# Performance work log

Measured on AMD Instinct MI355X. Metric: run time of the kernel, lower is better.

Reference implementation:

```python
import jax, jax.numpy as jnp
import numpy as np

C_IN = 64
C_QK = C_IN // 8  # 8


def setup_inputs() -> dict:
    key = jax.random.key(0)
    ks = jax.random.split(key, 8)
    B, C, D, H, W = 2, C_IN, 8, 32, 32
    x = jax.random.normal(ks[0], (B, C, D, H, W), dtype=jnp.float32)
    s = 1.0 / np.sqrt(C)
    Wq = jax.random.normal(ks[1], (C_QK, C), dtype=jnp.float32) * s
    bq = jax.random.normal(ks[2], (C_QK,), dtype=jnp.float32) * 0.01
    Wk = jax.random.normal(ks[3], (C_QK, C), dtype=jnp.float32) * s
    bk = jax.random.normal(ks[4], (C_QK,), dtype=jnp.float32) * 0.01
    Wv = jax.random.normal(ks[5], (C, C), dtype=jnp.float32) * s
    bv = jax.random.normal(ks[6], (C,), dtype=jnp.float32) * 0.01
    gamma = jax.random.normal(ks[7], (1,), dtype=jnp.float32) * 0.1
    return {"x": x, "Wq": Wq, "bq": bq, "Wk": Wk, "bk": bk,
            "Wv": Wv, "bv": bv, "gamma": gamma}


def reference(x, Wq, bq, Wk, bk, Wv, bv, gamma):
    B, C, D, H, W = x.shape
    N = D * H * W
    xf = x.reshape(B, C, N)  # flatten spatial dims (D,H,W order)
    # 1x1x1 conv3d == per-position channel matmul
    q = jnp.einsum('oc,bcn->bno', Wq, xf) + bq            # [B, N, Cqk]
    k = jnp.einsum('oc,bcn->bon', Wk, xf) + bk[:, None]   # [B, Cqk, N]
    v = jnp.einsum('oc,bcn->bon', Wv, xf) + bv[:, None]   # [B, C, N]
    energy = jnp.einsum('bnc,bcm->bnm', q, k)             # [B, N, N] (unscaled)
    attn = jax.nn.softmax(energy, axis=-1)
    # out[b,c,m] = sum_n v[b,c,n] * attn[b,m,n]  (bmm with attention^T)
    out = jnp.einsum('bcn,bmn->bcm', v, attn)
    out = out.reshape(B, C, D, H, W)
    return gamma[0] * out + x
```

## Files before the change

kernel.cpp:

```cpp
#include <hip/hip_runtime.h>
#include <hip/hip_bf16.h>
#include <math.h>

#define NPOS 8192
#define CIN 64
#define CQK 8
#define NB 2
#define LOG2E 1.4426950408889634f
#define SOFF 16.0f

typedef __attribute__((ext_vector_type(8))) short bf16x8;
typedef __attribute__((ext_vector_type(16))) float f32x16;

__device__ __forceinline__ unsigned short f2bf(float f) {
  union { float f; unsigned int u; } a; a.f = f;
  unsigned int r = a.u + 0x7FFFu + ((a.u >> 16) & 1u);
  return (unsigned short)(r >> 16);
}

__global__ __launch_bounds__(256, 2) void qkv_proj(
    const float* __restrict__ x,
    const float* __restrict__ Wq, const float* __restrict__ bq,
    const float* __restrict__ Wk, const float* __restrict__ bk,
    const float* __restrict__ Wv, const float* __restrict__ bv,
    unsigned short* __restrict__ Qb, unsigned short* __restrict__ Kb,
    unsigned short* __restrict__ VB) {
  __shared__ float sWq[CQK * CIN], sWk[CQK * CIN], sWv[CIN * CIN], sb[2 * CQK + CIN];
  __shared__ unsigned short sV[32][66];
  int t = threadIdx.x;
  for (int i = t; i < CQK * CIN; i += 256) { sWq[i] = Wq[i] * LOG2E; sWk[i] = Wk[i]; }
  for (int i = t; i < CIN * CIN; i += 256) sWv[i] = Wv[i];
  if (t < CQK) sb[t] = bq[t] * LOG2E;
  if (t >= CQK && t < 2 * CQK) sb[t] = bk[t - CQK];
  if (t >= 2 * CQK && t < 2 * CQK + CIN) sb[t] = bv[t - 2 * CQK];
  __syncthreads();

  int p_loc = t & 31, grp = t >> 5;
  int gid = blockIdx.x * 32 + p_loc;
  int b = gid >> 13;
  int n = gid & (NPOS - 1);
  const float* xp = x + (size_t)b * CIN * NPOS + n;
  float xv[CIN];
#pragma unroll
  for (int c = 0; c < CIN; ++c) xv[c] = xp[(size_t)c * NPOS];

  {
    int o = grp;
    float aq = sb[o], ak = sb[CQK + o];
    const float4* wq4 = (const float4*)&sWq[o * CIN];
    const float4* wk4 = (const float4*)&sWk[o * CIN];
#pragma unroll
    for (int c4 = 0; c4 < 16; ++c4) {
      float4 wq = wq4[c4], wk = wk4[c4];
      float x0 = xv[4 * c4], x1 = xv[4 * c4 + 1], x2 = xv[4 * c4 + 2], x3 = xv[4 * c4 + 3];
      aq += wq.x * x0 + wq.y * x1 + wq.z * x2 + wq.w * x3;
      ak += wk.x * x0 + wk.y * x1 + wk.z * x2 + wk.w * x3;
    }
    Qb[(size_t)gid * CQK + o] = f2bf(aq);
    Kb[(size_t)gid * CQK + o] = f2bf(ak);
  }
#pragma unroll
  for (int oo = 0; oo < 8; ++oo) {
    int o = grp * 8 + oo;
    float av = sb[2 * CQK + o];
    const float4* wv4 = (const float4*)&sWv[o * CIN];
#pragma unroll
    for (int c4 = 0; c4 < 16; ++c4) {
      float4 w = wv4[c4];
      av += w.x * xv[4 * c4] + w.y * xv[4 * c4 + 1] + w.z * xv[4 * c4 + 2] + w.w * xv[4 * c4 + 3];
    }
    sV[p_loc][o] = f2bf(av);
  }
  __syncthreads();

  {
    int gid0 = blockIdx.x * 32;
    int bb = gid0 >> 13;
    int jb = (gid0 & (NPOS - 1)) >> 5;
    int f = t >> 6;
    int ln = t & 63;
    int ch = ((f >> 1) << 5) + (ln & 31);
    int w0 = ((f & 1) << 4) + (((ln >> 5) & 1) << 2);
    union { unsigned short s[8]; bf16x8 v; } ou;
#pragma unroll
    for (int i = 0; i < 8; ++i) {
      int p = w0 + (i & 3) + (((i >> 2) & 1) << 3);
      ou.s[i] = sV[p][ch];
    }
    *reinterpret_cast<bf16x8*>(
        VB + (((size_t)bb * 256 + jb) * 2048 + (size_t)f * 512 + ln * 8)) = ou.v;
  }
}

__global__ __launch_bounds__(512, 2) void flash_attn(
    const unsigned short* __restrict__ Qb, const unsigned short* __restrict__ Kb,
    const unsigned short* __restrict__ VB, const float* __restrict__ x,
    const float* __restrict__ gamma, float* __restrict__ out) {
  int tid = threadIdx.x;
  int wave = tid >> 6, lane = tid & 63;
  int qcol = lane & 31, hi = lane >> 5;
  int blk = blockIdx.x;
  int b = blk >> 7, qt = blk & 127;
  int qbase = qt * 64;

  bf16x8 qfrag0, qfrag1;
#pragma unroll
  for (int i = 0; i < 8; ++i) { qfrag0[i] = 0; qfrag1[i] = 0; }
  if (!hi) {
    qfrag0 = *reinterpret_cast<const bf16x8*>(Qb + ((size_t)b * NPOS + qbase + qcol) * CQK);
    qfrag1 = *reinterpret_cast<const bf16x8*>(Qb + ((size_t)b * NPOS + qbase + 32 + qcol) * CQK);
  }

  f32x16 z;
#pragma unroll
  for (int i = 0; i < 16; ++i) z[i] = -SOFF;
  f32x16 accA0, accB0, accA1, accB1;
#pragma unroll
  for (int i = 0; i < 16; ++i) { accA0[i] = 0.f; accB0[i] = 0.f; accA1[i] = 0.f; accB1[i] = 0.f; }
  float l0 = 0.f, l1 = 0.f;

  const unsigned short* Kp = Kb + (size_t)b * NPOS * CQK;
  const bf16x8* Vt = reinterpret_cast<const bf16x8*>(VB + (size_t)b * 256 * 2048);

  int jb0 = wave << 5;
  bf16x8 kcur = *reinterpret_cast<const bf16x8*>(Kp + ((size_t)(jb0 << 5) + qcol) * CQK);

  for (int tt = 0; tt < 32; ++tt) {
    const bf16x8* tile = Vt + (size_t)(jb0 + tt) * 256;
    bf16x8 va0 = tile[lane];
    bf16x8 va1 = tile[64 + lane];
    bf16x8 vb0 = tile[128 + lane];
    bf16x8 vb1 = tile[192 + lane];

    f32x16 S0 = __builtin_amdgcn_mfma_f32_32x32x16_bf16(kcur, qfrag0, z, 0, 0, 0);
    f32x16 S1 = __builtin_amdgcn_mfma_f32_32x32x16_bf16(kcur, qfrag1, z, 0, 0, 0);

    int jn = jb0 + ((tt + 1) & 31);
    bf16x8 knx = *reinterpret_cast<const bf16x8*>(Kp + ((size_t)(jn << 5) + qcol) * CQK);

    unsigned int pk0[8], pk1[8];
    float lsa = 0.f, lsb = 0.f, lsc = 0.f, lsd = 0.f;
#pragma unroll
    for (int jj = 0; jj < 8; ++jj) {
      float pa = __builtin_amdgcn_exp2f(S0[2 * jj]);
      float pb = __builtin_amdgcn_exp2f(S0[2 * jj + 1]);
      float pc = __builtin_amdgcn_exp2f(S1[2 * jj]);
      float pd = __builtin_amdgcn_exp2f(S1[2 * jj + 1]);
      lsa += pa; lsb += pb; lsc += pc; lsd += pd;
      pk0[jj] = __builtin_amdgcn_perm(__float_as_uint(pb), __float_as_uint(pa), 0x07060302u);
      pk1[jj] = __builtin_amdgcn_perm(__float_as_uint(pd), __float_as_uint(pc), 0x07060302u);
    }
    l0 += lsa + lsb;
    l1 += lsc + lsd;

    union { unsigned int ui[4]; bf16x8 v; } PA00, PA10, PA01, PA11;
    PA00.ui[0] = pk0[0]; PA00.ui[1] = pk0[1]; PA00.ui[2] = pk0[2]; PA00.ui[3] = pk0[3];
    PA10.ui[0] = pk0[4]; PA10.ui[1] = pk0[5]; PA10.ui[2] = pk0[6]; PA10.ui[3] = pk0[7];
    PA01.ui[0] = pk1[0]; PA01.ui[1] = pk1[1]; PA01.ui[2] = pk1[2]; PA01.ui[3] = pk1[3];
    PA11.ui[0] = pk1[4]; PA11.ui[1] = pk1[5]; PA11.ui[2] = pk1[6]; PA11.ui[3] = pk1[7];

    accA0 = __builtin_amdgcn_mfma_f32_32x32x16_bf16(va0, PA00.v, accA0, 0, 0, 0);
    accA0 = __builtin_amdgcn_mfma_f32_32x32x16_bf16(va1, PA10.v, accA0, 0, 0, 0);
    accB0 = __builtin_amdgcn_mfma_f32_32x32x16_bf16(vb0, PA00.v, accB0, 0, 0, 0);
    accB0 = __builtin_amdgcn_mfma_f32_32x32x16_bf16(vb1, PA10.v, accB0, 0, 0, 0);
    accA1 = __builtin_amdgcn_mfma_f32_32x32x16_bf16(va0, PA01.v, accA1, 0, 0, 0);
    accA1 = __builtin_amdgcn_mfma_f32_32x32x16_bf16(va1, PA11.v, accA1, 0, 0, 0);
    accB1 = __builtin_amdgcn_mfma_f32_32x32x16_bf16(vb0, PA01.v, accB1, 0, 0, 0);
    accB1 = __builtin_amdgcn_mfma_f32_32x32x16_bf16(vb1, PA11.v, accB1, 0, 0, 0);

    kcur = knx;
  }

  __shared__ float sL[8][64];
  __shared__ float sLinv[64];
  __shared__ float sacc[64][68];
  float lp0 = l0 + __shfl_xor(l0, 32);
  float lp1 = l1 + __shfl_xor(l1, 32);
  if (!hi) { sL[wave][qcol] = lp0; sL[wave][32 + qcol] = lp1; }
  __syncthreads();
  if (tid < 64) {
    float L = 0.f;
#pragma unroll
    for (int w2 = 0; w2 < 8; ++w2) L += sL[w2][tid];
    sLinv[tid] = 1.0f / L;
  }

  for (int w2 = 0; w2 < 8; ++w2) {
    __syncthreads();
    if (wave == w2) {
#pragma unroll
      for (int k = 0; k < 4; ++k) {
        int c0 = (k << 3) + (hi << 2);
        float4 cA0 = make_float4(accA0[4 * k], accA0[4 * k + 1], accA0[4 * k + 2], accA0[4 * k + 3]);
        float4 cB0 = make_float4(accB0[4 * k], accB0[4 * k + 1], accB0[4 * k + 2], accB0[4 * k + 3]);
        float4 cA1 = make_float4(accA1[4 * k], accA1[4 * k + 1], accA1[4 * k + 2], accA1[4 * k + 3]);
        float4 cB1 = make_float4(accB1[4 * k], accB1[4 * k + 1], accB1[4 * k + 2], accB1[4 * k + 3]);
        float4* pA0 = (float4*)&sacc[qcol][c0];
        float4* pB0 = (float4*)&sacc[qcol][c0 + 32];
        float4* pA1 = (float4*)&sacc[32 + qcol][c0];
        float4* pB1 = (float4*)&sacc[32 + qcol][c0 + 32];
        if (w2 == 0) { *pA0 = cA0; *pB0 = cB0; *pA1 = cA1; *pB1 = cB1; }
        else {
          float4 a = *pA0, bb = *pB0, c = *pA1, d = *pB1;
          a.x += cA0.x; a.y += cA0.y; a.z += cA0.z; a.w += cA0.w;
          bb.x += cB0.x; bb.y += cB0.y; bb.z += cB0.z; bb.w += cB0.w;
          c.x += cA1.x; c.y += cA1.y; c.z += cA1.z; c.w += cA1.w;
          d.x += cB1.x; d.y += cB1.y; d.z += cB1.z; d.w += cB1.w;
          *pA0 = a; *pB0 = bb; *pA1 = c; *pB1 = d;
        }
      }
    }
  }
  __syncthreads();

  float g = gamma[0];
  for (int i = tid; i < CIN * 64; i += 512) {
    int c = i >> 6, q = i & 63;
    size_t idx = ((size_t)b * CIN + c) * NPOS + qbase + q;
    out[idx] = g * sacc[q][c] * sLinv[q] + x[idx];
  }
}

extern "C" void kernel_launch(void* const* d_in, const int* in_sizes, int n_in,
                              void* d_out, int out_size, void* d_ws, size_t ws_size,
                              hipStream_t stream) {
  const float* x     = (const float*)d_in[0];
  const float* Wq    = (const float*)d_in[1];
  const float* bq    = (const float*)d_in[2];
  const float* Wk    = (const float*)d_in[3];
  const float* bk    = (const float*)d_in[4];
  const float* Wv    = (const float*)d_in[5];
  const float* bv    = (const float*)d_in[6];
  const float* gamma = (const float*)d_in[7];
  float* out = (float*)d_out;

  unsigned short* Qb = (unsigned short*)d_ws;
  unsigned short* Kb = Qb + (size_t)NB * NPOS * CQK;
  unsigned short* VB = Kb + (size_t)NB * NPOS * CQK;

  qkv_proj<<<dim3(NB * NPOS / 32), dim3(256), 0, stream>>>(
      x, Wq, bq, Wk, bk, Wv, bv, Qb, Kb, VB);
  flash_attn<<<dim3(NB * NPOS / 64), dim3(512), 0, stream>>>(
      Qb, Kb, VB, x, gamma, out);
}
```

Baseline: 45.26 us.

## Fuse QKV projection and flash attention into one cooperative kernel with grid sync

Merges the projection kernel and the attention kernel into a single cooperative launch. Each 512-thread block projects 64 positions into Q/K/V workspace, then a grid-wide barrier separates the projection from the attention phase. This removes one kernel launch and the gap between kernels. In exchange it adds a grid-sync cost, requires all 256 blocks to be co-resident, and raises shared memory use per block.

```diff
diff --git a/kernel.cpp b/kernel.cpp
--- a/kernel.cpp
+++ b/kernel.cpp
@@ -1,6 +1,9 @@
 #include <hip/hip_runtime.h>
 #include <hip/hip_bf16.h>
+#include <hip/hip_cooperative_groups.h>
 #include <math.h>
+
+namespace cg = cooperative_groups;
 
 #define NPOS 8192
 #define CIN 64
@@ -18,84 +21,87 @@
   return (unsigned short)(r >> 16);
 }
 
-__global__ __launch_bounds__(256, 2) void qkv_proj(
+__global__ __launch_bounds__(512, 2) void pam_fused(
     const float* __restrict__ x,
     const float* __restrict__ Wq, const float* __restrict__ bq,
     const float* __restrict__ Wk, const float* __restrict__ bk,
     const float* __restrict__ Wv, const float* __restrict__ bv,
+    const float* __restrict__ gamma, float* __restrict__ out,
     unsigned short* __restrict__ Qb, unsigned short* __restrict__ Kb,
     unsigned short* __restrict__ VB) {
   __shared__ float sWq[CQK * CIN], sWk[CQK * CIN], sWv[CIN * CIN], sb[2 * CQK + CIN];
-  __shared__ unsigned short sV[32][66];
-  int t = threadIdx.x;
-  for (int i = t; i < CQK * CIN; i += 256) { sWq[i] = Wq[i] * LOG2E; sWk[i] = Wk[i]; }
-  for (int i = t; i < CIN * CIN; i += 256) sWv[i] = Wv[i];
-  if (t < CQK) sb[t] = bq[t] * LOG2E;
-  if (t >= CQK && t < 2 * CQK) sb[t] = bk[t - CQK];
-  if (t >= 2 * CQK && t < 2 * CQK + CIN) sb[t] = bv[t - 2 * CQK];
-  __syncthreads();
-
-  int p_loc = t & 31, grp = t >> 5;
-  int gid = blockIdx.x * 32 + p_loc;
-  int b = gid >> 13;
-  int n = gid & (NPOS - 1);
-  const float* xp = x + (size_t)b * CIN * NPOS + n;
-  float xv[CIN];
-#pragma unroll
-  for (int c = 0; c < CIN; ++c) xv[c] = xp[(size_t)c * NPOS];
-
+  __shared__ unsigned short sV[64][66];
   {
-    int o = grp;
-    float aq = sb[o], ak = sb[CQK + o];
-    const float4* wq4 = (const float4*)&sWq[o * CIN];
-    const float4* wk4 = (const float4*)&sWk[o * CIN];
-#pragma unroll
-    for (int c4 = 0; c4 < 16; ++c4) {
-      float4 wq = wq4[c4], wk = wk4[c4];
-      float x0 = xv[4 * c4], x1 = xv[4 * c4 + 1], x2 = xv[4 * c4 + 2], x3 = xv[4 * c4 + 3];
-      aq += wq.x * x0 + wq.y * x1 + wq.z * x2 + wq.w * x3;
-      ak += wk.x * x0 + wk.y * x1 + wk.z * x2 + wk.w * x3;
-    }
-    Qb[(size_t)gid * CQK + o] = f2bf(aq);
-    Kb[(size_t)gid * CQK + o] = f2bf(ak);
-  }
-#pragma unroll
-  for (int oo = 0; oo < 8; ++oo) {
-    int o = grp * 8 + oo;
-    float av = sb[2 * CQK + o];
-    const float4* wv4 = (const float4*)&sWv[o * CIN];
-#pragma unroll
-    for (int c4 = 0; c4 < 16; ++c4) {
-      float4 w = wv4[c4];
-      av += w.x * xv[4 * c4] + w.y * xv[4 * c4 + 1] + w.z * xv[4 * c4 + 2] + w.w * xv[4 * c4 + 3];
-    }
-    sV[p_loc][o] = f2bf(av);
-  }
-  __syncthreads();
-
-  {
-    int gid0 = blockIdx.x * 32;
-    int bb = gid0 >> 13;
-    int jb = (gid0 & (NPOS - 1)) >> 5;
-    int f = t >> 6;
-    int ln = t & 63;
-    int ch = ((f >> 1) << 5) + (ln & 31);
-    int w0 = ((f & 1) << 4) + (((ln >> 5) & 1) << 2);
-    union { unsigned short s[8]; bf16x8 v; } ou;
-#pragma unroll
-    for (int i = 0; i < 8; ++i) {
-      int p = w0 + (i & 3) + (((i >> 2) & 1) << 3);
-      ou.s[i] = sV[p][ch];
-    }
-    *reinterpret_cast<bf16x8*>(
-        VB + (((size_t)bb * 256 + jb) * 2048 + (size_t)f * 512 + ln * 8)) = ou.v;
-  }
-}
-
-__global__ __launch_bounds__(512, 2) void flash_attn(
-    const unsigned short* __restrict__ Qb, const unsigned short* __restrict__ Kb,
-    const unsigned short* __restrict__ VB, const float* __restrict__ x,
-    const float* __restrict__ gamma, float* __restrict__ out) {
+    int t = threadIdx.x;
+    for (int i = t; i < CQK * CIN; i += 512) { sWq[i] = Wq[i] * LOG2E; sWk[i] = Wk[i]; }
+    for (int i = t; i < CIN * CIN; i += 512) sWv[i] = Wv[i];
+    if (t < CQK) sb[t] = bq[t] * LOG2E;
+    if (t >= CQK && t < 2 * CQK) sb[t] = bk[t - CQK];
+    if (t >= 2 * CQK && t < 2 * CQK + CIN) sb[t] = bv[t - 2 * CQK];
+    __syncthreads();
+
+    int p_loc = t & 63, grp = t >> 6;
+    int gid = blockIdx.x * 64 + p_loc;
+    int b = gid >> 13;
+    int n = gid & (NPOS - 1);
+    const float* xp = x + (size_t)b * CIN * NPOS + n;
+    float xv[CIN];
+#pragma unroll
+    for (int c = 0; c < CIN; ++c) xv[c] = xp[(size_t)c * NPOS];
+
+    {
+      int o = grp;
+      float aq = sb[o], ak = sb[CQK + o];
+      const float4* wq4 = (const float4*)&sWq[o * CIN];
+      const float4* wk4 = (const float4*)&sWk[o * CIN];
+#pragma unroll
+      for (int c4 = 0; c4 < 16; ++c4) {
+        float4 wq = wq4[c4], wk = wk4[c4];
+        float x0 = xv[4 * c4], x1 = xv[4 * c4 + 1], x2 = xv[4 * c4 + 2], x3 = xv[4 * c4 + 3];
+        aq += wq.x * x0 + wq.y * x1 + wq.z * x2 + wq.w * x3;
+        ak += wk.x * x0 + wk.y * x1 + wk.z * x2 + wk.w * x3;
+      }
+      Qb[(size_t)gid * CQK + o] = f2bf(aq);
+      Kb[(size_t)gid * CQK + o] = f2bf(ak);
+    }
+#pragma unroll
+    for (int oo = 0; oo < 8; ++oo) {
+      int o = grp * 8 + oo;
+      float av = sb[2 * CQK + o];
+      const float4* wv4 = (const float4*)&sWv[o * CIN];
+#pragma unroll
+      for (int c4 = 0; c4 < 16; ++c4) {
+        float4 w = wv4[c4];
+        av += w.x * xv[4 * c4] + w.y * xv[4 * c4 + 1] + w.z * xv[4 * c4 + 2] + w.w * xv[4 * c4 + 3];
+      }
+      sV[p_loc][o] = f2bf(av);
+    }
+    __syncthreads();
+
+    {
+      int gid0 = blockIdx.x * 64;
+      int bb = gid0 >> 13;
+      int jb0 = (gid0 & (NPOS - 1)) >> 5;
+      int cc = t;
+      int jbl = cc >> 8;
+      int rem = cc & 255;
+      int f = rem >> 6;
+      int ln = rem & 63;
+      int ch = ((f >> 1) << 5) + (ln & 31);
+      int w0 = ((f & 1) << 4) + (((ln >> 5) & 1) << 2);
+      union { unsigned short s[8]; bf16x8 v; } ou;
+#pragma unroll
+      for (int i = 0; i < 8; ++i) {
+        int p = (jbl << 5) + w0 + (i & 3) + (((i >> 2) & 1) << 3);
+        ou.s[i] = sV[p][ch];
+      }
+      *reinterpret_cast<bf16x8*>(
+          VB + (((size_t)bb * 256 + jb0 + jbl) * 2048 + (size_t)f * 512 + ln * 8)) = ou.v;
+    }
+  }
+
+  cg::this_grid().sync();
+
   int tid = threadIdx.x;
   int wave = tid >> 6, lane = tid & 63;
   int qcol = lane & 31, hi = lane >> 5;
@@ -238,8 +244,9 @@
   unsigned short* Kb = Qb + (size_t)NB * NPOS * CQK;
   unsigned short* VB = Kb + (size_t)NB * NPOS * CQK;
 
-  qkv_proj<<<dim3(NB * NPOS / 32), dim3(256), 0, stream>>>(
-      x, Wq, bq, Wk, bk, Wv, bv, Qb, Kb, VB);
-  flash_attn<<<dim3(NB * NPOS / 64), dim3(512), 0, stream>>>(
-      Qb, Kb, VB, x, gamma, out);
+  void* args[] = {(void*)&x, (void*)&Wq, (void*)&bq, (void*)&Wk, (void*)&bk,
+                  (void*)&Wv, (void*)&bv, (void*)&gamma, (void*)&out,
+                  (void*)&Qb, (void*)&Kb, (void*)&VB};
+  hipLaunchCooperativeKernel((void*)pam_fused, dim3(NB * NPOS / 64), dim3(512),
+                             args, 0, stream);
 }
```

Measured after the change: 81.26 us. 79.5% more time.

## Replace exp2 with bit-trick approximation and compute row sums via MFMA

Applied to the files above, without the earlier changes.

Replaces the hardware exp2 in the softmax loop with a Schraudolph-style approximation: an FMA scales and biases the score, and the float-to-uint conversion yields the IEEE bit pattern, whose top 16 bits are packed straight into bf16. It also drops the per-lane scalar accumulation of softmax denominators and instead computes row sums with extra MFMAs against a vector of bf16 ones. This cuts transcendental and VALU work per tile but adds four MFMAs per iteration, and the exp approximation is far less accurate (piecewise-linear mantissa), which could hurt numerical correctness.

```diff
diff --git a/kernel.cpp b/kernel.cpp
--- a/kernel.cpp
+++ b/kernel.cpp
@@ -8,6 +8,8 @@
 #define NB 2
 #define LOG2E 1.4426950408889634f
 #define SOFF 16.0f
+#define EXP2_SCALE 8388608.0f
+#define EXP2_BIAS  1065173216.0f
 
 typedef __attribute__((ext_vector_type(8))) short bf16x8;
 typedef __attribute__((ext_vector_type(16))) float f32x16;
@@ -111,13 +113,20 @@
     qfrag1 = *reinterpret_cast<const bf16x8*>(Qb + ((size_t)b * NPOS + qbase + 32 + qcol) * CQK);
   }
 
+  bf16x8 ones;
+#pragma unroll
+  for (int i = 0; i < 8; ++i) ones[i] = (short)0x3F80;
+
   f32x16 z;
 #pragma unroll
   for (int i = 0; i < 16; ++i) z[i] = -SOFF;
   f32x16 accA0, accB0, accA1, accB1;
-#pragma unroll
-  for (int i = 0; i < 16; ++i) { accA0[i] = 0.f; accB0[i] = 0.f; accA1[i] = 0.f; accB1[i] = 0.f; }
-  float l0 = 0.f, l1 = 0.f;
+  f32x16 accL0, accL1;
+#pragma unroll
+  for (int i = 0; i < 16; ++i) {
+    accA0[i] = 0.f; accB0[i] = 0.f; accA1[i] = 0.f; accB1[i] = 0.f;
+    accL0[i] = 0.f; accL1[i] = 0.f;
+  }
 
   const unsigned short* Kp = Kb + (size_t)b * NPOS * CQK;
   const bf16x8* Vt = reinterpret_cast<const bf16x8*>(VB + (size_t)b * 256 * 2048);
@@ -139,19 +148,15 @@
     bf16x8 knx = *reinterpret_cast<const bf16x8*>(Kp + ((size_t)(jn << 5) + qcol) * CQK);
 
     unsigned int pk0[8], pk1[8];
-    float lsa = 0.f, lsb = 0.f, lsc = 0.f, lsd = 0.f;
 #pragma unroll
     for (int jj = 0; jj < 8; ++jj) {
-      float pa = __builtin_amdgcn_exp2f(S0[2 * jj]);
-      float pb = __builtin_amdgcn_exp2f(S0[2 * jj + 1]);
-      float pc = __builtin_amdgcn_exp2f(S1[2 * jj]);
-      float pd = __builtin_amdgcn_exp2f(S1[2 * jj + 1]);
-      lsa += pa; lsb += pb; lsc += pc; lsd += pd;
-      pk0[jj] = __builtin_amdgcn_perm(__float_as_uint(pb), __float_as_uint(pa), 0x07060302u);
-      pk1[jj] = __builtin_amdgcn_perm(__float_as_uint(pd), __float_as_uint(pc), 0x07060302u);
-    }
-    l0 += lsa + lsb;
-    l1 += lsc + lsd;
+      unsigned int ua = (unsigned int)fmaf(S0[2 * jj],     EXP2_SCALE, EXP2_BIAS);
+      unsigned int ub = (unsigned int)fmaf(S0[2 * jj + 1], EXP2_SCALE, EXP2_BIAS);
+      unsigned int uc = (unsigned int)fmaf(S1[2 * jj],     EXP2_SCALE, EXP2_BIAS);
+      unsigned int ud = (unsigned int)fmaf(S1[2 * jj + 1], EXP2_SCALE, EXP2_BIAS);
+      pk0[jj] = __builtin_amdgcn_perm(ub, ua, 0x07060302u);
+      pk1[jj] = __builtin_amdgcn_perm(ud, uc, 0x07060302u);
+    }
 
     union { unsigned int ui[4]; bf16x8 v; } PA00, PA10, PA01, PA11;
     PA00.ui[0] = pk0[0]; PA00.ui[1] = pk0[1]; PA00.ui[2] = pk0[2]; PA00.ui[3] = pk0[3];
@@ -167,6 +172,10 @@
     accA1 = __builtin_amdgcn_mfma_f32_32x32x16_bf16(va1, PA11.v, accA1, 0, 0, 0);
     accB1 = __builtin_amdgcn_mfma_f32_32x32x16_bf16(vb0, PA01.v, accB1, 0, 0, 0);
     accB1 = __builtin_amdgcn_mfma_f32_32x32x16_bf16(vb1, PA11.v, accB1, 0, 0, 0);
+    accL0 = __builtin_amdgcn_mfma_f32_32x32x16_bf16(ones, PA00.v, accL0, 0, 0, 0);
+    accL0 = __builtin_amdgcn_mfma_f32_32x32x16_bf16(ones, PA10.v, accL0, 0, 0, 0);
+    accL1 = __builtin_amdgcn_mfma_f32_32x32x16_bf16(ones, PA01.v, accL1, 0, 0, 0);
+    accL1 = __builtin_amdgcn_mfma_f32_32x32x16_bf16(ones, PA11.v, accL1, 0, 0, 0);
 
     kcur = knx;
   }
@@ -174,9 +183,7 @@
   __shared__ float sL[8][64];
   __shared__ float sLinv[64];
   __shared__ float sacc[64][68];
-  float lp0 = l0 + __shfl_xor(l0, 32);
-  float lp1 = l1 + __shfl_xor(l1, 32);
-  if (!hi) { sL[wave][qcol] = lp0; sL[wave][32 + qcol] = lp1; }
+  if (!hi) { sL[wave][qcol] = accL0[0]; sL[wave][32 + qcol] = accL1[0]; }
   __syncthreads();
   if (tid < 64) {
     float L = 0.f;
```

After: 46.21 us. 1.02x slower.

## Drop LDS weight staging in qkv_proj, read wave-uniform weights as scalars

Applied to the files above, without the earlier changes.

The projection kernel no longer copies Wq/Wk/Wv and biases into shared memory behind a block barrier. Each wave now owns one Q/K output and eight V outputs. Weights are indexed by a readfirstlane wave id, so they can be fetched as uniform scalar loads. The block grows to 512 threads covering 64 positions, and the V layout writeback is extended to two 32-position tiles. This removes the LDS fill and barrier cost, but relies on the scalar cache serving the weight reads and adds wave-uniform global loads inside unrolled loops.

```diff
diff --git a/kernel.cpp b/kernel.cpp
--- a/kernel.cpp
+++ b/kernel.cpp
@@ -18,25 +18,18 @@
   return (unsigned short)(r >> 16);
 }
 
-__global__ __launch_bounds__(256, 2) void qkv_proj(
+__global__ __launch_bounds__(512) void qkv_proj(
     const float* __restrict__ x,
     const float* __restrict__ Wq, const float* __restrict__ bq,
     const float* __restrict__ Wk, const float* __restrict__ bk,
     const float* __restrict__ Wv, const float* __restrict__ bv,
     unsigned short* __restrict__ Qb, unsigned short* __restrict__ Kb,
     unsigned short* __restrict__ VB) {
-  __shared__ float sWq[CQK * CIN], sWk[CQK * CIN], sWv[CIN * CIN], sb[2 * CQK + CIN];
-  __shared__ unsigned short sV[32][66];
-  int t = threadIdx.x;
-  for (int i = t; i < CQK * CIN; i += 256) { sWq[i] = Wq[i] * LOG2E; sWk[i] = Wk[i]; }
-  for (int i = t; i < CIN * CIN; i += 256) sWv[i] = Wv[i];
-  if (t < CQK) sb[t] = bq[t] * LOG2E;
-  if (t >= CQK && t < 2 * CQK) sb[t] = bk[t - CQK];
-  if (t >= 2 * CQK && t < 2 * CQK + CIN) sb[t] = bv[t - 2 * CQK];
-  __syncthreads();
-
-  int p_loc = t & 31, grp = t >> 5;
-  int gid = blockIdx.x * 32 + p_loc;
+  __shared__ unsigned short sV[64][66];
+  int tid = threadIdx.x;
+  int wave = __builtin_amdgcn_readfirstlane(tid >> 6);
+  int lane = tid & 63;
+  int gid = blockIdx.x * 64 + lane;
   int b = gid >> 13;
   int n = gid & (NPOS - 1);
   const float* xp = x + (size_t)b * CIN * NPOS + n;
@@ -45,50 +38,49 @@
   for (int c = 0; c < CIN; ++c) xv[c] = xp[(size_t)c * NPOS];
 
   {
-    int o = grp;
-    float aq = sb[o], ak = sb[CQK + o];
-    const float4* wq4 = (const float4*)&sWq[o * CIN];
-    const float4* wk4 = (const float4*)&sWk[o * CIN];
-#pragma unroll
-    for (int c4 = 0; c4 < 16; ++c4) {
-      float4 wq = wq4[c4], wk = wk4[c4];
-      float x0 = xv[4 * c4], x1 = xv[4 * c4 + 1], x2 = xv[4 * c4 + 2], x3 = xv[4 * c4 + 3];
-      aq += wq.x * x0 + wq.y * x1 + wq.z * x2 + wq.w * x3;
-      ak += wk.x * x0 + wk.y * x1 + wk.z * x2 + wk.w * x3;
-    }
-    Qb[(size_t)gid * CQK + o] = f2bf(aq);
-    Kb[(size_t)gid * CQK + o] = f2bf(ak);
+    const float* wq = Wq + wave * CIN;
+    const float* wk = Wk + wave * CIN;
+    float aq = 0.f, ak = 0.f;
+#pragma unroll
+    for (int c = 0; c < CIN; ++c) {
+      aq += wq[c] * xv[c];
+      ak += wk[c] * xv[c];
+    }
+    aq = (aq + bq[wave]) * LOG2E;
+    ak += bk[wave];
+    Qb[(size_t)gid * CQK + wave] = f2bf(aq);
+    Kb[(size_t)gid * CQK + wave] = f2bf(ak);
   }
 #pragma unroll
   for (int oo = 0; oo < 8; ++oo) {
-    int o = grp * 8 + oo;
-    float av = sb[2 * CQK + o];
-    const float4* wv4 = (const float4*)&sWv[o * CIN];
-#pragma unroll
-    for (int c4 = 0; c4 < 16; ++c4) {
-      float4 w = wv4[c4];
-      av += w.x * xv[4 * c4] + w.y * xv[4 * c4 + 1] + w.z * xv[4 * c4 + 2] + w.w * xv[4 * c4 + 3];
-    }
-    sV[p_loc][o] = f2bf(av);
+    int o = wave * 8 + oo;
+    const float* wv = Wv + o * CIN;
+    float av = bv[o];
+#pragma unroll
+    for (int c = 0; c < CIN; ++c) av += wv[c] * xv[c];
+    sV[lane][o] = f2bf(av);
   }
   __syncthreads();
 
   {
-    int gid0 = blockIdx.x * 32;
+    int gid0 = blockIdx.x * 64;
     int bb = gid0 >> 13;
-    int jb = (gid0 & (NPOS - 1)) >> 5;
-    int f = t >> 6;
-    int ln = t & 63;
+    int jb0 = (gid0 & (NPOS - 1)) >> 5;
+    int cc = tid;
+    int jbl = cc >> 8;
+    int rem = cc & 255;
+    int f = rem >> 6;
+    int ln = rem & 63;
     int ch = ((f >> 1) << 5) + (ln & 31);
     int w0 = ((f & 1) << 4) + (((ln >> 5) & 1) << 2);
     union { unsigned short s[8]; bf16x8 v; } ou;
 #pragma unroll
     for (int i = 0; i < 8; ++i) {
-      int p = w0 + (i & 3) + (((i >> 2) & 1) << 3);
+      int p = (jbl << 5) + w0 + (i & 3) + (((i >> 2) & 1) << 3);
       ou.s[i] = sV[p][ch];
     }
     *reinterpret_cast<bf16x8*>(
-        VB + (((size_t)bb * 256 + jb) * 2048 + (size_t)f * 512 + ln * 8)) = ou.v;
+        VB + (((size_t)bb * 256 + jb0 + jbl) * 2048 + (size_t)f * 512 + ln * 8)) = ou.v;
   }
 }
 
@@ -238,7 +230,7 @@
   unsigned short* Kb = Qb + (size_t)NB * NPOS * CQK;
   unsigned short* VB = Kb + (size_t)NB * NPOS * CQK;
 
-  qkv_proj<<<dim3(NB * NPOS / 32), dim3(256), 0, stream>>>(
+  qkv_proj<<<dim3(NB * NPOS / 64), dim3(512), 0, stream>>>(
       x, Wq, bq, Wk, bk, Wv, bv, Qb, Kb, VB);
   flash_attn<<<dim3(NB * NPOS / 64), dim3(512), 0, stream>>>(
       Qb, Kb, VB, x, gamma, out);
```

Measured after the change: 43.07 us (median of 3 runs). -4.8%, faster.
